# Kernel optimization log

Hardware: AMD Instinct MI355X
Metric: run time of the kernel (lower is better)

The kernel has to match this reference:

```python
import jax, jax.numpy as jnp
import numpy as np

N_HEAD = 16
N_EMBD = 1024

def setup_inputs() -> dict:
    key = jax.random.key(0)
    k1, k2, k3 = jax.random.split(key, 3)
    B, T, C = 4, 2048, N_EMBD
    x = jax.random.normal(k1, (B, T, C), dtype=jnp.float32)
    attention_mask = jnp.ones((B, T), dtype=jnp.int32)
    # nn.Linear(C, 3C, bias=False): y = x @ W_attn, stored as (C, 3C)
    W_attn = jax.random.normal(k2, (C, 3 * C), dtype=jnp.float32) * 0.02
    W_proj = jax.random.normal(k3, (C, C), dtype=jnp.float32) * 0.02
    return {"x": x, "attention_mask": attention_mask, "W_attn": W_attn, "W_proj": W_proj}

def reference(x, attention_mask, W_attn, W_proj):
    B, T, C = x.shape
    H = N_HEAD
    D = C // H
    qkv = x @ W_attn                                   # [B,T,3C]
    q, k, v = jnp.split(qkv, 3, axis=2)
    # [B,T,C] -> [B,H,T,D]
    q = q.reshape(B, T, H, D).transpose(0, 2, 1, 3)
    k = k.reshape(B, T, H, D).transpose(0, 2, 1, 3)
    v = v.reshape(B, T, H, D).transpose(0, 2, 1, 3)
    scale = 1.0 / jnp.sqrt(jnp.asarray(D, x.dtype))
    att = jnp.einsum('bhqd,bhkd->bhqk', q, k) * scale  # [B,H,T,T]
    causal = jnp.tril(jnp.ones((T, T), dtype=bool))    # [T,T]
    pad = attention_mask != 0                          # [B,T], key-side padding
    mask = causal[None, None, :, :] & pad[:, None, None, :]
    att = jnp.where(mask, att, -jnp.inf)
    att = jax.nn.softmax(att, axis=-1)
    # dropout=0.0 (eval): attn_dropout and resid_dropout are identity
    y = jnp.einsum('bhqk,bhkd->bhqd', att, v)          # [B,H,T,D]
    y = y.transpose(0, 2, 1, 3).reshape(B, T, C)
    return y @ W_proj
```

## Files before the change

kernel.cpp:

```cpp
#include <hip/hip_runtime.h>
#include <hip/hip_bf16.h>
#include <math.h>

#define TT 2048
#define CC 1024
#define C3 3072
#define MM 8192

typedef __attribute__((ext_vector_type(8))) short short8;
typedef __attribute__((ext_vector_type(4))) float f32x4;

__device__ __forceinline__ short bf16b(float x) {
  __hip_bfloat16 h = __float2bfloat16(x);
  return *reinterpret_cast<short*>(&h);
}

__device__ __forceinline__ unsigned cvtpk(float lo, float hi) {
  unsigned r;
  asm("v_cvt_pk_bf16_f32 %0, %1, %2" : "=v"(r) : "v"(lo), "v"(hi));
  return r;
}

__device__ __forceinline__ float exp2a(float x) {
  float r;
  asm("v_exp_f32 %0, %1" : "=v"(r) : "v"(x));
  return r;
}

__device__ __forceinline__ void gload16(const void* g, void* l) {
  __builtin_amdgcn_global_load_lds(
      (const __attribute__((address_space(1))) unsigned int*)g,
      (__attribute__((address_space(3))) unsigned int*)l, 16, 0, 0);
}

__device__ __forceinline__ void cvt_t_body(const float* __restrict__ in,
                                           short* __restrict__ out, int R, int Cc,
                                           int c0, int r0, int limit, float scale,
                                           float (*t)[33], int tid) {
  const int tx = tid & 31, ty = tid >> 5;
#pragma unroll
  for (int i = 0; i < 4; ++i)
    t[ty + i * 8][tx] = in[(size_t)(r0 + ty + i * 8) * Cc + c0 + tx];
  __syncthreads();
#pragma unroll
  for (int i = 0; i < 4; ++i) {
    const int orow = c0 + ty + i * 8;
    const float f = (orow < limit) ? scale : 1.f;
    out[(size_t)orow * R + r0 + tx] = bf16b(t[tx][ty + i * 8] * f);
  }
}

__global__ __launch_bounds__(256) void prep(const float* __restrict__ x,
                                            short* __restrict__ xb,
                                            const float* __restrict__ Wa,
                                            short* __restrict__ Wta,
                                            const float* __restrict__ Wp,
                                            short* __restrict__ Wtp,
                                            const int* __restrict__ amask,
                                            unsigned long long* __restrict__ kmask,
                                            float scaleQ) {
  __shared__ float t[32][33];
  const int bid = blockIdx.x, tid = threadIdx.x;
  if (bid < 4096) {
    const int i = (bid * 256 + tid) * 8;
    float4 a = *reinterpret_cast<const float4*>(x + i);
    float4 b = *reinterpret_cast<const float4*>(x + i + 4);
    short8 r;
    r[0] = bf16b(a.x); r[1] = bf16b(a.y); r[2] = bf16b(a.z); r[3] = bf16b(a.w);
    r[4] = bf16b(b.x); r[5] = bf16b(b.y); r[6] = bf16b(b.z); r[7] = bf16b(b.w);
    *reinterpret_cast<short8*>(xb + i) = r;
  } else if (bid < 7168) {
    const int lb = bid - 4096;
    cvt_t_body(Wa, Wta, CC, C3, (lb % 96) * 32, (lb / 96) * 32, CC, scaleQ, t, tid);
  } else if (bid < 8192) {
    const int lb = bid - 7168;
    cvt_t_body(Wp, Wtp, CC, CC, (lb & 31) * 32, (lb >> 5) * 32, 0, 1.f, t, tid);
  } else {
    const int gw = (bid - 8192) * 4 + (tid >> 6);
    unsigned long long bits = __ballot(amask[gw * 64 + (tid & 63)] != 0);
    if ((tid & 63) == 0) kmask[gw] = bits;
  }
}

template <int MODE>
__global__ __launch_bounds__(256) void gemm_bt(const short* __restrict__ A,
                                               const short* __restrict__ Bt,
                                               void* __restrict__ Cout,
                                               short* __restrict__ vT,
                                               int M, int N, int K) {
  __shared__ __align__(16) char Ls[2 * 32768];
  const int tid = threadIdx.x, lane = tid & 63, w = tid >> 6;
  const int g = lane >> 4, cw = lane & 15;
  const int m0 = blockIdx.y * 128, n0 = blockIdx.x * 128;
  const int wr = (w >> 1) * 64, wc = (w & 1) * 64;

  f32x4 acc[4][4];
#pragma unroll
  for (int i = 0; i < 4; ++i)
#pragma unroll
    for (int j = 0; j < 4; ++j) acc[i][j] = (f32x4){0.f, 0.f, 0.f, 0.f};

  const int sr = tid >> 3;
  const int sc = ((tid & 7) ^ (sr & 7)) << 3;
  const short* Asrc = A + (size_t)(m0 + sr) * K + sc;
  const short* Bsrc = Bt + (size_t)(n0 + sr) * K + sc;
  const size_t ustep = (size_t)32 * K;

  const int nt = K >> 6;

#define STAGE(kt, buf)                                                        \
  {                                                                           \
    char* dst_ = Ls + (buf) * 32768;                                          \
    const int k0_ = (kt) * 64;                                                \
    _Pragma("unroll")                                                         \
    for (int u = 0; u < 4; ++u)                                               \
      gload16(Asrc + u * ustep + k0_, dst_ + u * 4096 + tid * 16);            \
    _Pragma("unroll")                                                         \
    for (int u = 0; u < 4; ++u)                                               \
      gload16(Bsrc + u * ustep + k0_, dst_ + 16384 + u * 4096 + tid * 16);    \
  }

  STAGE(0, 0);
  STAGE(1, 1);

  const int xorm = (cw & 7) << 4;

#pragma unroll 1
  for (int t = 0; t < nt; ++t) {
    if (t + 1 < nt) {
      asm volatile("s_waitcnt vmcnt(8)" ::: "memory");
    } else {
      asm volatile("s_waitcnt vmcnt(0)" ::: "memory");
    }
    asm volatile("s_barrier" ::: "memory");

    const char* LA = Ls + (t & 1) * 32768;
    const char* LB = LA + 16384;

#pragma unroll
    for (int ks = 0; ks < 2; ++ks) {
      const int xo = (ks * 64 + g * 16) ^ xorm;
      short8 af[4], bf[4];
#pragma unroll
      for (int mt = 0; mt < 4; ++mt)
        af[mt] = *reinterpret_cast<const short8*>(LA + (wr + mt * 16 + cw) * 128 + xo);
#pragma unroll
      for (int ntn = 0; ntn < 4; ++ntn)
        bf[ntn] = *reinterpret_cast<const short8*>(LB + (wc + ntn * 16 + cw) * 128 + xo);
      __builtin_amdgcn_s_setprio(1);
#pragma unroll
      for (int mt = 0; mt < 4; ++mt)
#pragma unroll
        for (int ntn = 0; ntn < 4; ++ntn)
          acc[mt][ntn] = __builtin_amdgcn_mfma_f32_16x16x32_bf16(af[mt], bf[ntn], acc[mt][ntn], 0, 0, 0);
      __builtin_amdgcn_s_setprio(0);
    }

    asm volatile("s_barrier" ::: "memory");
    if (t + 2 < nt) STAGE(t + 2, t & 1);
  }
#undef STAGE

  if (MODE == 2 && n0 >= 2048) {
    char* Lt = Ls;
#pragma unroll
    for (int mt = 0; mt < 4; ++mt)
#pragma unroll
      for (int ntn = 0; ntn < 4; ++ntn) {
        const int dl = wc + ntn * 16 + cw;
        const int xm = (dl & 15) << 4;
        const int tl0 = wr + mt * 16 + g * 4;
        const int l5 = tl0 & 31;
        const int tp0 = (tl0 & ~31) | ((l5 & 8) << 1) | ((l5 & 4) << 1) |
                        ((l5 & 16) >> 2);
        uint2 v;
        v.x = cvtpk(acc[mt][ntn][0], acc[mt][ntn][1]);
        v.y = cvtpk(acc[mt][ntn][2], acc[mt][ntn][3]);
        *reinterpret_cast<uint2*>(Lt + dl * 256 + ((tp0 * 2) ^ xm)) = v;
      }
    __syncthreads();
    const int dl = tid >> 1, hf = tid & 1;
    const int b = m0 >> 11, t0 = m0 & 2047;
    const int h = ((n0 - 2048) >> 6) + (dl >> 6);
    const int d = dl & 63;
    short* dst = vT + (size_t)((b * 16 + h) * 64 + d) * TT + t0 + hf * 64;
#pragma unroll
    for (int c = 0; c < 8; ++c) {
      const int ca = hf * 8 + c;
      const int slot = ca ^ (dl & 15);
      *reinterpret_cast<short8*>(dst + c * 8) =
          *reinterpret_cast<const short8*>(Lt + dl * 256 + slot * 16);
    }
    return;
  }

#pragma unroll
  for (int mt = 0; mt < 4; ++mt)
#pragma unroll
    for (int ntn = 0; ntn < 4; ++ntn)
#pragma unroll
      for (int j = 0; j < 4; ++j) {
        int row = m0 + wr + mt * 16 + g * 4 + j;
        int col = n0 + wc + ntn * 16 + cw;
        if (MODE == 2)
          ((short*)Cout)[(size_t)row * N + col] = bf16b(acc[mt][ntn][j]);
        else
          ((float*)Cout)[(size_t)row * N + col] = acc[mt][ntn][j];
      }
}

__global__ __launch_bounds__(256, 4) void attn_mfma(const short* __restrict__ qkv,
                                                    const short* __restrict__ vT,
                                                    const unsigned long long* __restrict__ kmask,
                                                    short* __restrict__ y) {
  __shared__ __align__(16) char Ks[2 * 8192];
  __shared__ __align__(16) char Vs[2 * 8192];
  __shared__ unsigned long long km[32];
  const int tid = threadIdx.x, lane = tid & 63;
  const int w = tid >> 6;
  const int g = lane >> 4, cw = lane & 15;

  const int lin = blockIdx.y * 16 + blockIdx.x;
  const int swz = (lin & 7) * 128 + (lin >> 3);
  const int bh = swz >> 4, pr = swz & 15;
  const int b = bh >> 4, h = bh & 15;

  const int xorm = (cw & 7) << 4;
  const int srow = w * 8 + (lane >> 3);
  const int scb = (((lane & 7) ^ ((lane >> 3) & 7)) << 4);

  if (tid < 32) km[tid] = kmask[b * 32 + tid];

  const char* ksrc = (const char*)qkv + ((size_t)(b * TT + srow) * C3 + CC + h * 64) * 2 + scb;
  const char* vsrc = (const char*)vT + ((size_t)(bh * 64 + srow) * TT) * 2 + scb;

  const int kro = cw * 128;
  const int sz0 = (g * 16) ^ xorm;
  const int sz1 = (64 + g * 16) ^ xorm;

#pragma unroll 1
  for (int part = 0; part < 2; ++part) {
    const int qt = part ? 31 - pr : pr;
    const int qw = qt * 64 + w * 16;

    short8 qf[2];
#pragma unroll
    for (int ks = 0; ks < 2; ++ks)
      qf[ks] = *reinterpret_cast<const short8*>(
          &qkv[(size_t)(b * TT + qw + cw) * C3 + h * 64 + ks * 32 + g * 8]);

    f32x4 o[4];
#pragma unroll
    for (int nd = 0; nd < 4; ++nd) o[nd] = (f32x4){0.f, 0.f, 0.f, 0.f};
    float ls = 0.f;

    const int niter = qt + 1;
    const char* kp = ksrc;
    const char* vp = vsrc;
#pragma unroll
    for (int u = 0; u < 2; ++u) {
      gload16(kp + (size_t)(u * 32) * (C3 * 2), Ks + u * 4096 + tid * 16);
      gload16(vp + (size_t)(u * 32) * (TT * 2), Vs + u * 4096 + tid * 16);
    }

#pragma unroll 1
    for (int t = 0; t < niter; ++t) {
      const int cur = t & 1;
      if (t + 1 < niter) {
        kp += (size_t)64 * (C3 * 2);
        vp += 128;
        char* dK = Ks + (cur ^ 1) * 8192;
        char* dV = Vs + (cur ^ 1) * 8192;
#pragma unroll
        for (int u = 0; u < 2; ++u) {
          gload16(kp + (size_t)(u * 32) * (C3 * 2), dK + u * 4096 + tid * 16);
          gload16(vp + (size_t)(u * 32) * (TT * 2), dV + u * 4096 + tid * 16);
        }
        asm volatile("s_waitcnt vmcnt(4)" ::: "memory");
      } else {
        asm volatile("s_waitcnt vmcnt(0)" ::: "memory");
      }
      asm volatile("s_barrier" ::: "memory");

      const int kbase = t * 64;
      if (kbase <= qw + 15) {
        const char* KB = Ks + cur * 8192;
        const char* VB = Vs + cur * 8192;

        f32x4 s[4];
        __builtin_amdgcn_s_setprio(1);
#pragma unroll
        for (int nt = 0; nt < 4; ++nt) {
          short8 kf0 = *reinterpret_cast<const short8*>(KB + nt * 2048 + kro + sz0);
          short8 kf1 = *reinterpret_cast<const short8*>(KB + nt * 2048 + kro + sz1);
          f32x4 z = (f32x4){0.f, 0.f, 0.f, 0.f};
          s[nt] = __builtin_amdgcn_mfma_f32_16x16x32_bf16(kf0, qf[0], z, 0, 0, 0);
          s[nt] = __builtin_amdgcn_mfma_f32_16x16x32_bf16(kf1, qf[1], s[nt], 0, 0, 0);
        }
        __builtin_amdgcn_s_setprio(0);

        const unsigned long long kb = km[t];
        if ((kbase + 63 > qw) || (kb != ~0ULL)) {
          const int q = qw + cw;
#pragma unroll
          for (int nt = 0; nt < 4; ++nt)
#pragma unroll
            for (int j = 0; j < 4; ++j) {
              const int kh = nt * 16 + g * 4 + j;
              const bool mok = (kb >> kh) & 1;
              if (!(mok && kbase + kh <= q)) s[nt][j] = -1e30f;
            }
        }

        float rs = 0.f;
#pragma unroll
        for (int nt = 0; nt < 4; ++nt)
#pragma unroll
          for (int j = 0; j < 4; ++j) {
            const float p = exp2a(s[nt][j]);
            s[nt][j] = p;
            rs += p;
          }
        ls += rs;

        short8 pa[2];
#pragma unroll
        for (int ks2 = 0; ks2 < 2; ++ks2) {
          union { unsigned u[4]; short8 s8; } pc;
          pc.u[0] = cvtpk(s[2 * ks2][0], s[2 * ks2][1]);
          pc.u[1] = cvtpk(s[2 * ks2][2], s[2 * ks2][3]);
          pc.u[2] = cvtpk(s[2 * ks2 + 1][0], s[2 * ks2 + 1][1]);
          pc.u[3] = cvtpk(s[2 * ks2 + 1][2], s[2 * ks2 + 1][3]);
          pa[ks2] = pc.s8;
        }

        __builtin_amdgcn_s_setprio(1);
#pragma unroll
        for (int ks2 = 0; ks2 < 2; ++ks2)
#pragma unroll
          for (int nd = 0; nd < 4; ++nd) {
            short8 vf = *reinterpret_cast<const short8*>(
                VB + nd * 2048 + kro + (ks2 ? sz1 : sz0));
            o[nd] = __builtin_amdgcn_mfma_f32_16x16x32_bf16(pa[ks2], vf, o[nd], 0, 0, 0);
          }
        __builtin_amdgcn_s_setprio(0);
      }
      asm volatile("s_barrier" ::: "memory");
    }

    ls += __shfl_xor(ls, 16);
    ls += __shfl_xor(ls, 32);
#pragma unroll
    for (int j = 0; j < 4; ++j) {
      const float lj = __shfl(ls, (lane & 48) | (g * 4 + j));
      const float inv = 1.f / lj;
      const int q = qw + g * 4 + j;
#pragma unroll
      for (int nd = 0; nd < 4; ++nd)
        y[(size_t)(b * TT + q) * CC + h * 64 + nd * 16 + cw] = bf16b(o[nd][j] * inv);
    }
  }
}

extern "C" void kernel_launch(void* const* d_in, const int* in_sizes, int n_in,
                              void* d_out, int out_size, void* d_ws, size_t ws_size,
                              hipStream_t stream) {
  const float* x      = (const float*)d_in[0];
  const int*   amask  = (const int*)d_in[1];
  const float* W_attn = (const float*)d_in[2];
  const float* W_proj = (const float*)d_in[3];

  char* ws = (char*)d_ws;
  short* xb  = (short*)(ws);
  short* Wta = (short*)(ws + 16777216);
  short* Wtp = (short*)(ws + 23068672);
  short* qkv = (short*)(ws + 25165824);
  short* y   = (short*)(ws + 75497472);
  short* vT  = (short*)(ws + 92274688);
  unsigned long long* kmask = (unsigned long long*)(ws + 109051904);

  const float SC = 0.18033688011112043f;

  prep<<<8224, 256, 0, stream>>>(x, xb, W_attn, Wta, W_proj, Wtp, amask, kmask, SC);
  {
    dim3 g(C3 / 128, MM / 128);
    gemm_bt<2><<<g, 256, 0, stream>>>(xb, Wta, qkv, vT, MM, C3, CC);
  }
  {
    dim3 g(16, 64);
    attn_mfma<<<g, 256, 0, stream>>>(qkv, vT, kmask, y);
  }
  {
    dim3 g(CC / 128, MM / 128);
    gemm_bt<0><<<g, 256, 0, stream>>>(y, Wtp, (void*)d_out, nullptr, MM, CC, CC);
  }
}
```

Measured before the change: 152.9 us.

## Split attention into one block per query tile, drop double buffering, raise occupancy

```diff
diff --git a/kernel.cpp b/kernel.cpp
--- a/kernel.cpp
+++ b/kernel.cpp
@@ -209,20 +209,19 @@
       }
 }
 
-__global__ __launch_bounds__(256, 4) void attn_mfma(const short* __restrict__ qkv,
+__global__ __launch_bounds__(256, 8) void attn_mfma(const short* __restrict__ qkv,
                                                     const short* __restrict__ vT,
                                                     const unsigned long long* __restrict__ kmask,
                                                     short* __restrict__ y) {
-  __shared__ __align__(16) char Ks[2 * 8192];
-  __shared__ __align__(16) char Vs[2 * 8192];
+  __shared__ __align__(16) char Ks[8192];
+  __shared__ __align__(16) char Vs[8192];
   __shared__ unsigned long long km[32];
   const int tid = threadIdx.x, lane = tid & 63;
   const int w = tid >> 6;
   const int g = lane >> 4, cw = lane & 15;
 
-  const int lin = blockIdx.y * 16 + blockIdx.x;
-  const int swz = (lin & 7) * 128 + (lin >> 3);
-  const int bh = swz >> 4, pr = swz & 15;
+  const int qt = 31 - ((int)blockIdx.x >> 6);
+  const int bh = blockIdx.x & 63;
   const int b = bh >> 4, h = bh & 15;
 
   const int xorm = (cw & 7) << 4;
@@ -238,127 +237,102 @@
   const int sz0 = (g * 16) ^ xorm;
   const int sz1 = (64 + g * 16) ^ xorm;
 
+  const int qw = qt * 64 + w * 16;
+
+  short8 qf[2];
+#pragma unroll
+  for (int ks = 0; ks < 2; ++ks)
+    qf[ks] = *reinterpret_cast<const short8*>(
+        &qkv[(size_t)(b * TT + qw + cw) * C3 + h * 64 + ks * 32 + g * 8]);
+
+  f32x4 o[4];
+#pragma unroll
+  for (int nd = 0; nd < 4; ++nd) o[nd] = (f32x4){0.f, 0.f, 0.f, 0.f};
+  float ls = 0.f;
+
+  const int niter = qt + 1;
 #pragma unroll 1
-  for (int part = 0; part < 2; ++part) {
-    const int qt = part ? 31 - pr : pr;
-    const int qw = qt * 64 + w * 16;
-
-    short8 qf[2];
-#pragma unroll
-    for (int ks = 0; ks < 2; ++ks)
-      qf[ks] = *reinterpret_cast<const short8*>(
-          &qkv[(size_t)(b * TT + qw + cw) * C3 + h * 64 + ks * 32 + g * 8]);
-
-    f32x4 o[4];
-#pragma unroll
-    for (int nd = 0; nd < 4; ++nd) o[nd] = (f32x4){0.f, 0.f, 0.f, 0.f};
-    float ls = 0.f;
-
-    const int niter = qt + 1;
-    const char* kp = ksrc;
-    const char* vp = vsrc;
+  for (int t = 0; t < niter; ++t) {
+    __syncthreads();
 #pragma unroll
     for (int u = 0; u < 2; ++u) {
-      gload16(kp + (size_t)(u * 32) * (C3 * 2), Ks + u * 4096 + tid * 16);
-      gload16(vp + (size_t)(u * 32) * (TT * 2), Vs + u * 4096 + tid * 16);
-    }
-
-#pragma unroll 1
-    for (int t = 0; t < niter; ++t) {
-      const int cur = t & 1;
-      if (t + 1 < niter) {
-        kp += (size_t)64 * (C3 * 2);
-        vp += 128;
-        char* dK = Ks + (cur ^ 1) * 8192;
-        char* dV = Vs + (cur ^ 1) * 8192;
-#pragma unroll
-        for (int u = 0; u < 2; ++u) {
-          gload16(kp + (size_t)(u * 32) * (C3 * 2), dK + u * 4096 + tid * 16);
-          gload16(vp + (size_t)(u * 32) * (TT * 2), dV + u * 4096 + tid * 16);
+      gload16(ksrc + (size_t)(t * 64) * (C3 * 2) + (size_t)(u * 32) * (C3 * 2),
+              Ks + u * 4096 + tid * 16);
+      gload16(vsrc + (size_t)(u * 32) * (TT * 2) + (size_t)t * 128,
+              Vs + u * 4096 + tid * 16);
+    }
+    __syncthreads();
+
+    f32x4 s[4];
+    __builtin_amdgcn_s_setprio(1);
+#pragma unroll
+    for (int nt = 0; nt < 4; ++nt) {
+      short8 kf0 = *reinterpret_cast<const short8*>(Ks + nt * 2048 + kro + sz0);
+      short8 kf1 = *reinterpret_cast<const short8*>(Ks + nt * 2048 + kro + sz1);
+      f32x4 z = (f32x4){0.f, 0.f, 0.f, 0.f};
+      s[nt] = __builtin_amdgcn_mfma_f32_16x16x32_bf16(kf0, qf[0], z, 0, 0, 0);
+      s[nt] = __builtin_amdgcn_mfma_f32_16x16x32_bf16(kf1, qf[1], s[nt], 0, 0, 0);
+    }
+    __builtin_amdgcn_s_setprio(0);
+
+    const int kbase = t * 64;
+    const unsigned long long kb = km[t];
+    if ((kbase + 63 > qw) || (kb != ~0ULL)) {
+      const int q = qw + cw;
+#pragma unroll
+      for (int nt = 0; nt < 4; ++nt)
+#pragma unroll
+        for (int j = 0; j < 4; ++j) {
+          const int kh = nt * 16 + g * 4 + j;
+          const bool mok = (kb >> kh) & 1;
+          if (!(mok && kbase + kh <= q)) s[nt][j] = -1e30f;
         }
-        asm volatile("s_waitcnt vmcnt(4)" ::: "memory");
-      } else {
-        asm volatile("s_waitcnt vmcnt(0)" ::: "memory");
+    }
+
+    float rs = 0.f;
+#pragma unroll
+    for (int nt = 0; nt < 4; ++nt)
+#pragma unroll
+      for (int j = 0; j < 4; ++j) {
+        const float p = exp2a(s[nt][j]);
+        s[nt][j] = p;
+        rs += p;
       }
-      asm volatile("s_barrier" ::: "memory");
-
-      const int kbase = t * 64;
-      if (kbase <= qw + 15) {
-        const char* KB = Ks + cur * 8192;
-        const char* VB = Vs + cur * 8192;
-
-        f32x4 s[4];
-        __builtin_amdgcn_s_setprio(1);
-#pragma unroll
-        for (int nt = 0; nt < 4; ++nt) {
-          short8 kf0 = *reinterpret_cast<const short8*>(KB + nt * 2048 + kro + sz0);
-          short8 kf1 = *reinterpret_cast<const short8*>(KB + nt * 2048 + kro + sz1);
-          f32x4 z = (f32x4){0.f, 0.f, 0.f, 0.f};
-          s[nt] = __builtin_amdgcn_mfma_f32_16x16x32_bf16(kf0, qf[0], z, 0, 0, 0);
-          s[nt] = __builtin_amdgcn_mfma_f32_16x16x32_bf16(kf1, qf[1], s[nt], 0, 0, 0);
-        }
-        __builtin_amdgcn_s_setprio(0);
-
-        const unsigned long long kb = km[t];
-        if ((kbase + 63 > qw) || (kb != ~0ULL)) {
-          const int q = qw + cw;
-#pragma unroll
-          for (int nt = 0; nt < 4; ++nt)
-#pragma unroll
-            for (int j = 0; j < 4; ++j) {
-              const int kh = nt * 16 + g * 4 + j;
-              const bool mok = (kb >> kh) & 1;
-              if (!(mok && kbase + kh <= q)) s[nt][j] = -1e30f;
-            }
-        }
-
-        float rs = 0.f;
-#pragma unroll
-        for (int nt = 0; nt < 4; ++nt)
-#pragma unroll
-          for (int j = 0; j < 4; ++j) {
-            const float p = exp2a(s[nt][j]);
-            s[nt][j] = p;
-            rs += p;
-          }
-        ls += rs;
-
-        short8 pa[2];
-#pragma unroll
-        for (int ks2 = 0; ks2 < 2; ++ks2) {
-          union { unsigned u[4]; short8 s8; } pc;
-          pc.u[0] = cvtpk(s[2 * ks2][0], s[2 * ks2][1]);
-          pc.u[1] = cvtpk(s[2 * ks2][2], s[2 * ks2][3]);
-          pc.u[2] = cvtpk(s[2 * ks2 + 1][0], s[2 * ks2 + 1][1]);
-          pc.u[3] = cvtpk(s[2 * ks2 + 1][2], s[2 * ks2 + 1][3]);
-          pa[ks2] = pc.s8;
-        }
-
-        __builtin_amdgcn_s_setprio(1);
-#pragma unroll
-        for (int ks2 = 0; ks2 < 2; ++ks2)
-#pragma unroll
-          for (int nd = 0; nd < 4; ++nd) {
-            short8 vf = *reinterpret_cast<const short8*>(
-                VB + nd * 2048 + kro + (ks2 ? sz1 : sz0));
-            o[nd] = __builtin_amdgcn_mfma_f32_16x16x32_bf16(pa[ks2], vf, o[nd], 0, 0, 0);
-          }
-        __builtin_amdgcn_s_setprio(0);
+    ls += rs;
+
+    short8 pa[2];
+#pragma unroll
+    for (int ks2 = 0; ks2 < 2; ++ks2) {
+      union { unsigned u[4]; short8 s8; } pc;
+      pc.u[0] = cvtpk(s[2 * ks2][0], s[2 * ks2][1]);
+      pc.u[1] = cvtpk(s[2 * ks2][2], s[2 * ks2][3]);
+      pc.u[2] = cvtpk(s[2 * ks2 + 1][0], s[2 * ks2 + 1][1]);
+      pc.u[3] = cvtpk(s[2 * ks2 + 1][2], s[2 * ks2 + 1][3]);
+      pa[ks2] = pc.s8;
+    }
+
+    __builtin_amdgcn_s_setprio(1);
+#pragma unroll
+    for (int ks2 = 0; ks2 < 2; ++ks2)
+#pragma unroll
+      for (int nd = 0; nd < 4; ++nd) {
+        short8 vf = *reinterpret_cast<const short8*>(
+            Vs + nd * 2048 + kro + (ks2 ? sz1 : sz0));
+        o[nd] = __builtin_amdgcn_mfma_f32_16x16x32_bf16(pa[ks2], vf, o[nd], 0, 0, 0);
       }
-      asm volatile("s_barrier" ::: "memory");
-    }
-
-    ls += __shfl_xor(ls, 16);
-    ls += __shfl_xor(ls, 32);
-#pragma unroll
-    for (int j = 0; j < 4; ++j) {
-      const float lj = __shfl(ls, (lane & 48) | (g * 4 + j));
-      const float inv = 1.f / lj;
-      const int q = qw + g * 4 + j;
-#pragma unroll
-      for (int nd = 0; nd < 4; ++nd)
-        y[(size_t)(b * TT + q) * CC + h * 64 + nd * 16 + cw] = bf16b(o[nd][j] * inv);
-    }
+    __builtin_amdgcn_s_setprio(0);
+  }
+
+  ls += __shfl_xor(ls, 16);
+  ls += __shfl_xor(ls, 32);
+#pragma unroll
+  for (int j = 0; j < 4; ++j) {
+    const float lj = __shfl(ls, (lane & 48) | (g * 4 + j));
+    const float inv = 1.f / lj;
+    const int q = qw + g * 4 + j;
+#pragma unroll
+    for (int nd = 0; nd < 4; ++nd)
+      y[(size_t)(b * TT + q) * CC + h * 64 + nd * 16 + cw] = bf16b(o[nd][j] * inv);
   }
 }
 
@@ -386,10 +360,7 @@
     dim3 g(C3 / 128, MM / 128);
     gemm_bt<2><<<g, 256, 0, stream>>>(xb, Wta, qkv, vT, MM, C3, CC);
   }
-  {
-    dim3 g(16, 64);
-    attn_mfma<<<g, 256, 0, stream>>>(qkv, vT, kmask, y);
-  }
+  attn_mfma<<<2048, 256, 0, stream>>>(qkv, vT, kmask, y);
   {
     dim3 g(CC / 128, MM / 128);
     gemm_bt<0><<<g, 256, 0, stream>>>(y, Wtp, (void*)d_out, nullptr, MM, CC, CC);
```

Measured after the change: 170.8 us. 11.7% more time.
